# Optimization experiments

Hardware: AMD Instinct MI355X
Metric: run time of the kernel (lower is better)

## Reference

```python
import jax, jax.numpy as jnp
import numpy as np

N, F_IN, H, OUT, E = 50000, 128, 128, 40, 800000


def setup_inputs() -> dict:
    key = jax.random.key(0)
    ks = jax.random.split(key, 20)
    s = 0.05
    return {
        "x": jax.random.normal(ks[0], (N, F_IN), jnp.float32),
        "edge_index": jax.random.randint(ks[1], (2, E), 0, N, jnp.int64),
        # GATConv (heads=1)
        "W_gat": jax.random.normal(ks[2], (F_IN, H), jnp.float32) * s,
        "att_src": jax.random.normal(ks[3], (H,), jnp.float32) * s,
        "att_dst": jax.random.normal(ks[4], (H,), jnp.float32) * s,
        "b_gat": jnp.zeros((H,), jnp.float32),
        # GCNConv
        "W_gcn": jax.random.normal(ks[5], (F_IN, H), jnp.float32) * s,
        "b_gcn": jnp.zeros((H,), jnp.float32),
        # SAGEConv (mean aggr): lin_l on neighbors (with bias), lin_r on root (no bias)
        "W_sage_l": jax.random.normal(ks[6], (F_IN, H), jnp.float32) * s,
        "b_sage_l": jnp.zeros((H,), jnp.float32),
        "W_sage_r": jax.random.normal(ks[7], (F_IN, H), jnp.float32) * s,
        # MLP head
        "W1": jax.random.normal(ks[8], (3 * H, 2 * H), jnp.float32) * s,
        "b1": jnp.zeros((2 * H,), jnp.float32),
        "W2": jax.random.normal(ks[9], (2 * H, H), jnp.float32) * s,
        "b2": jnp.zeros((H,), jnp.float32),
        "W3": jax.random.normal(ks[10], (H, OUT), jnp.float32) * s,
        "b3": jnp.zeros((OUT,), jnp.float32),
        # BatchNorm1d(3H)
        "gamma": jnp.ones((3 * H,), jnp.float32),
        "beta": jnp.zeros((3 * H,), jnp.float32),
    }


def _add_self_loops(edge_index, n):
    loop = jnp.arange(n, dtype=edge_index.dtype)
    src = jnp.concatenate([edge_index[0], loop])
    dst = jnp.concatenate([edge_index[1], loop])
    return src, dst


def _gat(x, src, dst, n, W, att_src, att_dst, bias):
    h = x @ W                                   # [N, H]
    a_s = h @ att_src                           # [N]
    a_d = h @ att_dst                           # [N]
    e = jax.nn.leaky_relu(a_s[src] + a_d[dst], 0.2)  # [E']
    m = jax.ops.segment_max(e, dst, num_segments=n)
    ex = jnp.exp(e - m[dst])
    denom = jax.ops.segment_sum(ex, dst, num_segments=n)
    alpha = ex / denom[dst]
    out = jax.ops.segment_sum(alpha[:, None] * h[src], dst, num_segments=n)
    return out + bias


def _gcn(x, src, dst, n, W, bias):
    h = x @ W
    deg = jax.ops.segment_sum(jnp.ones_like(dst, dtype=h.dtype), dst, num_segments=n)
    dinv = jnp.where(deg > 0, jax.lax.rsqrt(deg), 0.0)
    norm = dinv[src] * dinv[dst]                # [E']
    out = jax.ops.segment_sum(norm[:, None] * h[src], dst, num_segments=n)
    return out + bias


def _sage(x, src, dst, n, W_l, b_l, W_r):
    agg = jax.ops.segment_sum(x[src], dst, num_segments=n)
    cnt = jax.ops.segment_sum(jnp.ones_like(dst, dtype=x.dtype), dst, num_segments=n)
    mean = agg / jnp.maximum(cnt, 1.0)[:, None]
    return mean @ W_l + b_l + x @ W_r


def reference(x, edge_index, W_gat, att_src, att_dst, b_gat, W_gcn, b_gcn,
              W_sage_l, b_sage_l, W_sage_r, W1, b1, W2, b2, W3, b3, gamma, beta):
    n = x.shape[0]
    src, dst = edge_index[0], edge_index[1]          # SAGE: no self-loops
    src_sl, dst_sl = _add_self_loops(edge_index, n)  # GAT/GCN add self-loops

    x_gat = _gat(x, src_sl, dst_sl, n, W_gat, att_src, att_dst, b_gat)
    x_gcn = _gcn(x, src_sl, dst_sl, n, W_gcn, b_gcn)
    x_sage = _sage(x, src, dst, n, W_sage_l, b_sage_l, W_sage_r)

    h = jnp.concatenate([x_gat, x_gcn, x_sage], axis=1)  # [N, 3H]
    # BatchNorm1d (training-mode batch statistics; biased variance, eps=1e-5)
    mu = h.mean(axis=0)
    var = h.var(axis=0)
    h = (h - mu) * jax.lax.rsqrt(var + 1e-5) * gamma + beta
    # dropout is identity at inference
    h = jax.nn.relu(h) @ W1 + b1
    h = jax.nn.relu(h) @ W2 + b2
    h = jax.nn.relu(h) @ W3 + b3
    return h
```

## Files before the change

### kernel.cpp

```cpp
#include <hip/hip_runtime.h>
#include <cstdint>
#include <cstddef>

#define NN   50000
#define FIN  128
#define HD   128
#define EE   800000
#define C3   384
#define NOUT 40

#define NBLK ((NN + 127) / 128)

#define SPLIT_BLKS ((NN + 4) / 4)

#define NBUCK ((NN + 511) / 512)
#define BCAP  16384
#define BK_BLKS ((EE + 8191) / 8192)
#define SCAP  12288

#define RCAP      132
#define STORE_CAP 128
#define ZROW NN

#define LDSW 132

typedef __attribute__((ext_vector_type(8))) short s8v;
typedef __attribute__((ext_vector_type(4))) float f4v;
typedef __attribute__((ext_vector_type(8))) ushort u8v;

typedef const __attribute__((address_space(1))) unsigned int* guintp;
typedef __attribute__((address_space(3))) unsigned int* luintp;

static __device__ __forceinline__ void async_copy16(const void* g, void* l) {
    __builtin_amdgcn_global_load_lds((guintp)g, (luintp)l, 16, 0, 0);
}

static __device__ __forceinline__ float b2f(ushort u) {
    return __uint_as_float((unsigned)u << 16);
}
static __device__ __forceinline__ ushort f2b(float v) {
    unsigned u = __float_as_uint(v);
    unsigned r = u + 0x7fffu + ((u >> 16) & 1u);
    return (ushort)(r >> 16);
}

__global__ __launch_bounds__(256) void k_split_x_att(
    const float* __restrict__ x,
    const float* __restrict__ w_as, const float* __restrict__ w_ad,
    ushort* __restrict__ xb,
    float* __restrict__ a_s, float* __restrict__ a_d)
{
    int node = blockIdx.x * 4 + (threadIdx.x >> 6);
    if (node > NN) return;
    int lane = threadIdx.x & 63;
    size_t o = (size_t)node * 128 + lane * 2;
    if (node == NN) {
        ushort2 z; z.x = 0; z.y = 0;
        *(ushort2*)(xb + o) = z;
        return;
    }
    float2 v  = *(const float2*)(x + o);
    { ushort2 u; u.x = f2b(v.x); u.y = f2b(v.y); *(ushort2*)(xb + o) = u; }
    float2 w1 = *(const float2*)(w_as + lane * 2);
    float2 w2 = *(const float2*)(w_ad + lane * 2);
    float s1 = v.x * w1.x + v.y * w1.y;
    float s2 = v.x * w2.x + v.y * w2.y;
    #pragma unroll
    for (int off = 32; off; off >>= 1) {
        s1 += __shfl_down(s1, off);
        s2 += __shfl_down(s2, off);
    }
    if (lane == 0) { a_s[node] = s1; a_d[node] = s2; }
}

__global__ void k_splitw_all(
    const float* __restrict__ Wg, const float* __restrict__ Wc,
    const float* __restrict__ Wl, const float* __restrict__ Wr,
    const float* __restrict__ W1, const float* __restrict__ W2,
    const float* __restrict__ W3,
    const float* __restrict__ asv, const float* __restrict__ adv,
    float* __restrict__ w_as, float* __restrict__ w_ad,
    ushort* __restrict__ btg, ushort* __restrict__ btc,
    ushort* __restrict__ btsg,
    ushort* __restrict__ bt1, ushort* __restrict__ bt2,
    ushort* __restrict__ bt3)
{
    int ry = blockIdx.x;
    int t = threadIdx.x;
    if (ry == 816) {
        if (t < 128) {
            float s1 = 0.f, s2 = 0.f;
            for (int j = 0; j < 128; ++j) {
                float w = Wg[t * 128 + j];
                s1 += w * asv[j];
                s2 += w * adv[j];
            }
            w_as[t] = s1; w_ad[t] = s2;
        }
        return;
    }
    const float* W = nullptr; ushort* dh; int K, Nw, n;
    bool sage = false;
    if (ry < 128)      { n = ry;       K = 128; Nw = 128; W = Wg; dh = btg; }
    else if (ry < 256) { n = ry - 128; K = 128; Nw = 128; W = Wc; dh = btc; }
    else if (ry < 384) { n = ry - 256; K = 256; Nw = 128; sage = true; dh = btsg; }
    else if (ry < 640) { n = ry - 384; K = 384; Nw = 256; W = W1; dh = bt1; }
    else if (ry < 768) { n = ry - 640; K = 256; Nw = 128; W = W2; dh = bt2; }
    else               { n = ry - 768; K = 128; Nw = 40;  W = W3; dh = bt3; }
    for (int k = t; k < K; k += 256) {
        float v;
        if (sage) v = (k < 128) ? Wl[(size_t)k * 128 + n] : Wr[(size_t)(k - 128) * 128 + n];
        else      v = (n < Nw) ? W[(size_t)k * Nw + n] : 0.f;
        dh[(size_t)n * K + k] = f2b(v);
    }
}

template<int NT, int NCH, int AX>
__global__ __launch_bounds__(256, 5) void k_gemm2(
    const ushort* __restrict__ A, int K,
    const ushort* __restrict__ Bt,
    int M, int mode,
    const float* __restrict__ bias,
    float* __restrict__ Cf, int ldc,
    ushort* __restrict__ Ch, int ldch,
    int colmax)
{
    constexpr int COLS = NT * 16;
    constexpr int HOPU = 8 * COLS;
    constexpr int KTOT = NCH * 128;

    __shared__ __align__(16) ushort S[16384];
    ushort* Bs = S;
    ushort* As = S + 8192;

    const int lane = threadIdx.x & 63;
    const int wave = threadIdx.x >> 6;
    const int quad = lane >> 4;
    const int ln15 = lane & 15;
    const int brow = AX ? blockIdx.y : blockIdx.x;
    const int bcol = AX ? blockIdx.x : blockIdx.y;
    const int row0 = brow * 128 + wave * 32;
    const int col0 = bcol * COLS;
    const int Rbase = brow * 128;

    auto stageB = [&](int c, int h) {
        for (int u0 = wave * 64; u0 < HOPU; u0 += 256) {
            int u  = u0 + lane;
            int kq  = u / COLS;
            int col = u - kq * COLS;
            int kk  = c * 128 + h * 64 + kq * 8;
            const ushort* gp = Bt + (size_t)(col0 + col) * KTOT + kk;
            async_copy16(gp, (char*)Bs + (size_t)u0 * 16);
        }
    };
    auto stageA = [&](int c, int h) {
        #pragma unroll
        for (int i = 0; i < 4; ++i) {
            int u0 = (wave * 4 + i) * 64;
            int u  = u0 + lane;
            int row = u >> 3;
            int s   = u & 7;
            int sg  = s ^ (row & 7);
            int rr = Rbase + row; if (rr > M - 1) rr = M - 1;
            int kk = c * 128 + h * 64 + sg * 8;
            const ushort* gp = A + (size_t)rr * K + kk;
            async_copy16(gp, (char*)As + (size_t)u0 * 16);
        }
    };
    auto afrag = [&](int jj, int mt) -> s8v {
        int r = wave * 32 + mt * 16 + ln15;
        int sg = jj * 4 + quad;
        int unit = r * 8 + (sg ^ (r & 7));
        return *(const s8v*)(As + (size_t)unit * 8);
    };

    f4v acc[2][NT] = {};

    auto compute = [&](int jj) {
        s8v a0 = afrag(jj, 0);
        s8v a1 = afrag(jj, 1);
        #pragma unroll
        for (int t = 0; t < NT; ++t) {
            int ub = (jj * 4 + quad) * COLS + t * 16 + ln15;
            s8v b = *(const s8v*)(Bs + (size_t)ub * 8);
            acc[0][t] = __builtin_amdgcn_mfma_f32_16x16x32_bf16(a0, b, acc[0][t], 0, 0, 0);
            acc[1][t] = __builtin_amdgcn_mfma_f32_16x16x32_bf16(a1, b, acc[1][t], 0, 0, 0);
        }
    };

    stageB(0, 0); stageA(0, 0);
    __syncthreads();

    #pragma unroll
    for (int ph = 0; ph < NCH; ++ph) {
        #pragma unroll
        for (int h = 0; h < 2; ++h) {
            compute(0); compute(1);
            if (!(ph == NCH - 1 && h == 1)) {
                __syncthreads();
                int nc = ph, nh = h + 1;
                if (nh == 2) { nh = 0; ++nc; }
                stageB(nc, nh); stageA(nc, nh);
                __syncthreads();
            }
        }
    }

    if (NT == 8 && mode == 0) {
        __syncthreads();
        ushort* Lp = S + wave * 2176;
        #pragma unroll
        for (int mt = 0; mt < 2; ++mt) {
            #pragma unroll
            for (int t = 0; t < NT; ++t) {
                int cc = col0 + t * 16 + ln15;
                #pragma unroll
                for (int r = 0; r < 4; ++r) {
                    float v = acc[mt][t][r] + bias[cc];
                    v = v > 0.f ? v : 0.f;
                    Lp[(quad * 4 + r) * LDSW + t * 16 + ln15] = f2b(v);
                }
            }
            int cb = (lane & 31) * 4;
            #pragma unroll
            for (int it = 0; it < 8; ++it) {
                int row2 = it * 2 + (lane >> 5);
                int rr = row0 + mt * 16 + row2;
                uint2 v = *(uint2*)(Lp + row2 * LDSW + cb);
                if (rr < M)
                    *(uint2*)(Ch + (size_t)rr * ldch + col0 + cb) = v;
            }
        }
    } else {
        #pragma unroll
        for (int t = 0; t < NT; ++t) {
            int cc = col0 + t * 16 + ln15;
            #pragma unroll
            for (int mt = 0; mt < 2; ++mt) {
                #pragma unroll
                for (int r = 0; r < 4; ++r) {
                    int rr = row0 + mt * 16 + quad * 4 + r;
                    if (rr < M && cc < colmax)
                        Cf[(size_t)rr * ldc + cc] = acc[mt][t][r] + bias[cc];
                }
            }
        }
    }
}

__global__ __launch_bounds__(256, 3) void k_gemm_prod(
    const ushort* __restrict__ tgb, const ushort* __restrict__ tcb,
    const ushort* __restrict__ tsb, const ushort* __restrict__ xb,
    const ushort* __restrict__ btg, const ushort* __restrict__ btc,
    const ushort* __restrict__ btsg,
    const float* __restrict__ bg, const float* __restrict__ bc,
    const float* __restrict__ bsl,
    float* __restrict__ pS, float* __restrict__ pQ,
    ushort* __restrict__ hch)
{
    constexpr int COLS = 128;
    constexpr int HOPU = 8 * COLS;
    __shared__ __align__(16) ushort S[16384];
    ushort* Bs = S;
    ushort* As = S + 8192;
    float* red = (float*)(S + 14336);

    const int z = blockIdx.z;
    const ushort* A1 = (z == 0) ? tgb : (z == 1) ? tcb : tsb;
    const ushort* Bt = (z == 0) ? btg : (z == 1) ? btc : btsg;
    const float*  bias = (z == 0) ? bg : (z == 1) ? bc : bsl;
    const int nch = (z == 2) ? 2 : 1;
    const int ktot = nch * 128;

    const int lane = threadIdx.x & 63;
    const int wave = threadIdx.x >> 6;
    const int quad = lane >> 4;
    const int ln15 = lane & 15;
    const int row0 = blockIdx.x * 128 + wave * 32;
    const int Rbase = blockIdx.x * 128;

    auto stageB = [&](int c, int h) {
        for (int u0 = wave * 64; u0 < HOPU; u0 += 256) {
            int u  = u0 + lane;
            int kq  = u / COLS;
            int col = u - kq * COLS;
            int kk  = c * 128 + h * 64 + kq * 8;
            const ushort* gp = Bt + (size_t)col * ktot + kk;
            async_copy16(gp, (char*)Bs + (size_t)u0 * 16);
        }
    };
    auto stageA = [&](int c, int h) {
        #pragma unroll
        for (int i = 0; i < 4; ++i) {
            int u0 = (wave * 4 + i) * 64;
            int u  = u0 + lane;
            int row = u >> 3;
            int s   = u & 7;
            int sg  = s ^ (row & 7);
            int rr = Rbase + row; if (rr > NN - 1) rr = NN - 1;
            int kk = c * 128 + h * 64 + sg * 8;
            const ushort* gp = (kk < 128) ? (A1 + (size_t)rr * 128 + kk)
                                          : (xb + (size_t)rr * 128 + (kk - 128));
            async_copy16(gp, (char*)As + (size_t)u0 * 16);
        }
    };
    auto afrag = [&](int jj, int mt) -> s8v {
        int r = wave * 32 + mt * 16 + ln15;
        int sg = jj * 4 + quad;
        int unit = r * 8 + (sg ^ (r & 7));
        return *(const s8v*)(As + (size_t)unit * 8);
    };

    f4v acc[2][8] = {};

    auto compute = [&](int jj) {
        s8v a0 = afrag(jj, 0);
        s8v a1 = afrag(jj, 1);
        #pragma unroll
        for (int t = 0; t < 8; ++t) {
            int ub = (jj * 4 + quad) * COLS + t * 16 + ln15;
            s8v b = *(const s8v*)(Bs + (size_t)ub * 8);
            acc[0][t] = __builtin_amdgcn_mfma_f32_16x16x32_bf16(a0, b, acc[0][t], 0, 0, 0);
            acc[1][t] = __builtin_amdgcn_mfma_f32_16x16x32_bf16(a1, b, acc[1][t], 0, 0, 0);
        }
    };

    stageB(0, 0); stageA(0, 0);
    __syncthreads();

    for (int ph = 0; ph < nch; ++ph) {
        for (int h = 0; h < 2; ++h) {
            compute(0); compute(1);
            if (!(ph == nch - 1 && h == 1)) {
                __syncthreads();
                int nc = ph, nh = h + 1;
                if (nh == 2) { nh = 0; ++nc; }
                stageB(nc, nh); stageA(nc, nh);
                __syncthreads();
            }
        }
    }

    __syncthreads();
    if (threadIdx.x < 256) red[threadIdx.x] = 0.f;
    ushort* Lp = S + wave * 2176;
    float sp[8] = {}, qp[8] = {};
    #pragma unroll
    for (int mt = 0; mt < 2; ++mt) {
        #pragma unroll
        for (int t = 0; t < 8; ++t) {
            #pragma unroll
            for (int r = 0; r < 4; ++r) {
                int rr = row0 + mt * 16 + quad * 4 + r;
                float v = acc[mt][t][r] + bias[t * 16 + ln15];
                Lp[(quad * 4 + r) * LDSW + t * 16 + ln15] = f2b(v);
                if (rr < NN) { sp[t] += v; qp[t] += v * v; }
            }
        }
        int cb = (lane & 31) * 4;
        #pragma unroll
        for (int it = 0; it < 8; ++it) {
            int row2 = it * 2 + (lane >> 5);
            int rr = row0 + mt * 16 + row2;
            uint2 v = *(uint2*)(Lp + row2 * LDSW + cb);
            if (rr < NN)
                *(uint2*)(hch + (size_t)rr * C3 + z * 128 + cb) = v;
        }
    }
    __syncthreads();
    #pragma unroll
    for (int t = 0; t < 8; ++t) {
        float s = sp[t], q = qp[t];
        s += __shfl_xor(s, 16); s += __shfl_xor(s, 32);
        q += __shfl_xor(q, 16); q += __shfl_xor(q, 32);
        if (quad == 0) {
            atomicAdd(&red[t * 16 + ln15], s);
            atomicAdd(&red[128 + t * 16 + ln15], q);
        }
    }
    __syncthreads();
    if (threadIdx.x < 128) {
        size_t o = (size_t)blockIdx.x * C3 + z * 128 + threadIdx.x;
        pS[o] = red[threadIdx.x];
        pQ[o] = red[128 + threadIdx.x];
    }
}

__global__ __launch_bounds__(1024) void k_bucket(
    const int* __restrict__ e_src, const int* __restrict__ e_dst,
    int* __restrict__ bcnt, uint* __restrict__ ebuf)
{
    __shared__ uint sval[8192];
    __shared__ int scnt[NBUCK], sbase[NBUCK];
    int t = threadIdx.x;
    if (t < NBUCK) scnt[t] = 0;
    __syncthreads();
    int e0 = blockIdx.x * 8192;
    #pragma unroll
    for (int i = 0; i < 8; ++i) {
        int g = e0 + i * 1024 + t;
        uint val = 0xffffffffu;
        if (g < EE) {
            int d = e_dst[g];
            int s = e_src[g];
            int b = d >> 9;
            val = ((uint)b << 25) | ((uint)(d & 511) << 16) | (uint)s;
            atomicAdd(&scnt[b], 1);
        }
        sval[i * 1024 + t] = val;
    }
    __syncthreads();
    if (t < NBUCK) {
        sbase[t] = atomicAdd(&bcnt[t], scnt[t]);
        scnt[t] = 0;
    }
    __syncthreads();
    #pragma unroll
    for (int i = 0; i < 8; ++i) {
        uint val = sval[i * 1024 + t];
        if (val != 0xffffffffu) {
            int b = val >> 25;
            int lo = atomicAdd(&scnt[b], 1);
            ebuf[(size_t)b * BCAP + sbase[b] + lo] = val;
        }
    }
}

__global__ __launch_bounds__(1024) void k_degscan(
    const int* __restrict__ bcnt, const uint* __restrict__ ebuf,
    int* __restrict__ offs, float* __restrict__ dinv)
{
    __shared__ int hist[512];
    __shared__ int sh[256];
    __shared__ int btop;
    int b = blockIdx.x, t = threadIdx.x;
    int d0 = b * 512;
    if (t < 512) hist[t] = 0;
    __syncthreads();
    int nb = bcnt[b];
    const uint* eb = ebuf + (size_t)b * BCAP;
    for (int i = t; i < nb; i += 1024)
        atomicAdd(&hist[(eb[i] >> 16) & 511], 1);
    __syncthreads();
    if (t < 64) {
        int acc = 0;
        for (int i = t; i < b; i += 64) {
            int nd = NN - i * 512; if (nd > 512) nd = 512;
            acc += bcnt[i] + nd;
        }
        #pragma unroll
        for (int off = 32; off; off >>= 1) acc += __shfl_down(acc, off);
        if (t == 0) btop = acc;
    }
    int v0 = 0, v1 = 0;
    if (t < 256) {
        int i0g = d0 + t * 2;
        v0 = (i0g < NN) ? hist[t * 2] + 1 : 0;
        v1 = (i0g + 1 < NN) ? hist[t * 2 + 1] + 1 : 0;
        sh[t] = v0 + v1;
    }
    __syncthreads();
    for (int off = 1; off < 256; off <<= 1) {
        int u = 0;
        if (t < 256 && t >= off) u = sh[t - off];
        __syncthreads();
        if (t < 256) sh[t] += u;
        __syncthreads();
    }
    if (t < 256) {
        int pair = v0 + v1;
        int excl = sh[t] - pair + btop;
        int i0g = d0 + t * 2;
        if (i0g < NN)     { offs[i0g] = excl;          dinv[i0g] = rsqrtf((float)v0); }
        if (i0g + 1 < NN) { offs[i0g + 1] = excl + v0; dinv[i0g + 1] = rsqrtf((float)v1); }
        if (b == NBUCK - 1 && t == 255) offs[NN] = excl + pair;
    }
}

__global__ __launch_bounds__(1024) void k_csr_build(
    const int* __restrict__ bcnt, const uint* __restrict__ ebuf,
    const int* __restrict__ offs, ushort* __restrict__ esrc)
{
    __shared__ ushort sout[SCAP];
    __shared__ int cur[512];
    int b = blockIdx.x, t = threadIdx.x;
    int d0 = b * 512;
    int ndst = NN - d0; if (ndst > 512) ndst = 512;
    int obase = offs[d0];
    if (t < ndst) cur[t] = offs[d0 + t] - obase;
    __syncthreads();
    int nb = bcnt[b];
    const uint* eb = ebuf + (size_t)b * BCAP;
    for (int i = t; i < nb; i += 1024) {
        uint val = eb[i];
        int slot = atomicAdd(&cur[(val >> 16) & 511], 1);
        sout[slot] = (ushort)(val & 0xffffu);
    }
    if (t < ndst) {
        int slot = atomicAdd(&cur[t], 1);
        sout[slot] = (ushort)(d0 + t);
    }
    __syncthreads();
    int total = offs[d0 + ndst] - obase;
    for (int i = t; i < total; i += 1024)
        esrc[obase + i] = sout[i];
}

__global__ __launch_bounds__(256) void k_gather(
    const ushort* __restrict__ esrc, const int* __restrict__ offs,
    const float* __restrict__ a_s, const float* __restrict__ a_d,
    const float* __restrict__ dinv,
    const ushort* __restrict__ xb,
    ushort* __restrict__ tgb, ushort* __restrict__ tcb,
    ushort* __restrict__ tsb)
{
    __shared__ uint2 recs[16][RCAP];
    int t = threadIdx.x;
    int qid = t >> 4;
    int ln = t & 15;
    int d = blockIdx.x * 16 + qid;
    if (d >= NN) return;
    uint2* rec = recs[qid];
    int beg = offs[d], end = offs[d + 1];
    int cnt = end - beg;
    float ad = a_d[d], dd = dinv[d];
    int stored = cnt < STORE_CAP ? cnt : STORE_CAP;

    float mloc = -3.0e38f;
    for (int b = 0; b < cnt; b += 16) {
        int j = b + ln;
        if (j < cnt) {
            int s = esrc[beg + j];
            float e = a_s[s] + ad;
            e = (e > 0.f) ? e : 0.2f * e;
            mloc = fmaxf(mloc, e);
            if (j < STORE_CAP) {
                uint2 r;
                r.x = __float_as_uint(e);
                r.y = (uint)s | ((uint)f2b(dinv[s] * dd) << 16);
                rec[j] = r;
            }
        }
    }
    float m = mloc;
    #pragma unroll
    for (int off = 1; off < 16; off <<= 1) m = fmaxf(m, __shfl_xor(m, off, 16));

    float denl = 0.f;
    for (int j = ln; j < stored; j += 16) {
        float ex = expf(__uint_as_float(rec[j].x) - m);
        denl += ex;
        rec[j].x = __float_as_uint(ex);
    }
    for (int idx = beg + STORE_CAP + ln; idx < end; idx += 16) {
        int s = esrc[idx];
        float e = a_s[s] + ad;
        e = (e > 0.f) ? e : 0.2f * e;
        denl += expf(e - m);
    }
    float den = denl;
    #pragma unroll
    for (int off = 1; off < 16; off <<= 1) den += __shfl_xor(den, off, 16);
    float rden = 1.f / den;

    for (int j = ln; j < stored; j += 16) {
        uint2 r = rec[j];
        uint2 q;
        q.x = (uint)f2b(__uint_as_float(r.x) * rden) | (r.y & 0xffff0000u);
        q.y = r.y & 0xffffu;
        rec[j] = q;
    }
    if (ln < 2) { uint2 q; q.x = 0u; q.y = (uint)ZROW; rec[stored + ln] = q; }

    float tg[8] = {}, tc[8] = {}, ts[8] = {};
    const ushort* xbs = xb + ln * 8;
    auto ldx = [&](uint srow) -> u8v {
        return *(const u8v*)(xbs + (size_t)srow * 128);
    };
    auto fmacc = [&](u8v x8, uint pw) {
        float wg = __uint_as_float(pw << 16);
        float wc = __uint_as_float(pw & 0xffff0000u);
        #pragma unroll
        for (int k = 0; k < 8; ++k) {
            float xv = b2f(x8[k]);
            tg[k] += wg * xv;
            tc[k] += wc * xv;
            ts[k] += xv;
        }
    };

    int Pcnt = (stored + 1) & ~1;
    uint2 rA = rec[0]; u8v xA = ldx(rA.y);
    uint2 rB; u8v xB;
    int j = 0;
    for (;;) {
        rB = rec[j + 1]; xB = ldx(rB.y);
        fmacc(xA, rA.x);
        if (++j >= Pcnt) break;
        rA = rec[j + 1]; xA = ldx(rA.y);
        fmacc(xB, rB.x);
        if (++j >= Pcnt) break;
    }

    for (int base = beg + STORE_CAP; base < end; base += 16) {
        int idx = base + ln;
        int s = ZROW; uint pw = 0;
        if (idx < end) {
            int ss = esrc[idx];
            float e = a_s[ss] + ad;
            e = (e > 0.f) ? e : 0.2f * e;
            pw = (uint)f2b(expf(e - m) * rden) | ((uint)f2b(dinv[ss] * dd) << 16);
            s = ss;
        }
        int cb = end - base; if (cb > 16) cb = 16;
        for (int jj = 0; jj < cb; ++jj) {
            int sa = __shfl(s, jj, 16);
            uint pa = (uint)__shfl((int)pw, jj, 16);
            fmacc(ldx((uint)sa), pa);
        }
    }

    u8v xd = *(const u8v*)(xb + (size_t)d * 128 + ln * 8);
    int cs = cnt - 1;
    float rc = 1.f / (float)(cs > 1 ? cs : 1);
    u8v og, oc, os;
    #pragma unroll
    for (int k = 0; k < 8; ++k) {
        og[k] = f2b(tg[k]);
        oc[k] = f2b(tc[k]);
        os[k] = f2b((ts[k] - b2f(xd[k])) * rc);
    }
    size_t row = (size_t)d * 128 + ln * 8;
    *(u8v*)(tgb + row) = og;
    *(u8v*)(tcb + row) = oc;
    *(u8v*)(tsb + row) = os;
}

__global__ void k_bn_final(const float* __restrict__ pS, const float* __restrict__ pQ,
                           const float* __restrict__ gamma, const float* __restrict__ beta,
                           float* __restrict__ scale, float* __restrict__ shift)
{
    int j = blockIdx.x * 64 + threadIdx.x;
    if (j >= C3) return;
    float s = 0.f, q = 0.f;
    for (int r = 0; r < NBLK; ++r) {
        s += pS[(size_t)r * C3 + j];
        q += pQ[(size_t)r * C3 + j];
    }
    const float rn = 1.f / (float)NN;
    float mu  = s * rn;
    float var = q * rn - mu * mu;
    float sc  = gamma[j] * rsqrtf(var + 1e-5f);
    scale[j] = sc;
    shift[j] = beta[j] - mu * sc;
}

__global__ __launch_bounds__(256) void k_bnrelu(
    ushort* __restrict__ hch,
    const float* __restrict__ scale, const float* __restrict__ shift)
{
    int p = blockIdx.x * blockDim.x + threadIdx.x;
    if (p >= NN * 48) return;
    int cidx = (p % 48) * 8;
    size_t o = (size_t)p * 8;
    uint4 w = *(uint4*)(hch + o);
    uint wr[4] = {w.x, w.y, w.z, w.w};
    uint out[4];
    #pragma unroll
    for (int i = 0; i < 4; ++i) {
        ushort u0 = (ushort)(wr[i] & 0xffffu), u1 = (ushort)(wr[i] >> 16);
        int cc = cidx + i * 2;
        float v0 = b2f(u0) * scale[cc]     + shift[cc];
        float v1 = b2f(u1) * scale[cc + 1] + shift[cc + 1];
        v0 = v0 > 0.f ? v0 : 0.f;
        v1 = v1 > 0.f ? v1 : 0.f;
        out[i] = (uint)f2b(v0) | ((uint)f2b(v1) << 16);
    }
    uint4 r; r.x = out[0]; r.y = out[1]; r.z = out[2]; r.w = out[3];
    *(uint4*)(hch + o) = r;
}

extern "C" void kernel_launch(void* const* d_in, const int* in_sizes, int n_in,
                              void* d_out, int out_size, void* d_ws, size_t ws_size,
                              hipStream_t stream) {
    const float* x        = (const float*)d_in[0];
    const int*   ei       = (const int*)d_in[1];
    const float* W_gat    = (const float*)d_in[2];
    const float* att_src  = (const float*)d_in[3];
    const float* att_dst  = (const float*)d_in[4];
    const float* b_gat    = (const float*)d_in[5];
    const float* W_gcn    = (const float*)d_in[6];
    const float* b_gcn    = (const float*)d_in[7];
    const float* W_sage_l = (const float*)d_in[8];
    const float* b_sage_l = (const float*)d_in[9];
    const float* W_sage_r = (const float*)d_in[10];
    const float* W1       = (const float*)d_in[11];
    const float* b1       = (const float*)d_in[12];
    const float* W2       = (const float*)d_in[13];
    const float* b2       = (const float*)d_in[14];
    const float* W3       = (const float*)d_in[15];
    const float* b3       = (const float*)d_in[16];
    const float* gamma    = (const float*)d_in[17];
    const float* beta     = (const float*)d_in[18];

    const int* e_src = ei;
    const int* e_dst = ei + EE;

    char* base = (char*)d_ws;
    size_t o = 0;
    ushort* hch  = (ushort*)(base + o); o += (size_t)NN * C3 * 2;
    ushort* tgb  = (ushort*)(base + o); o += (size_t)NN * 128 * 2;
    ushort* tcb  = (ushort*)(base + o); o += (size_t)NN * 128 * 2;
    ushort* tsb  = (ushort*)(base + o); o += (size_t)NN * 128 * 2;
    ushort* xb   = (ushort*)(base + o); o += (size_t)(NN + 1) * 128 * 2;
    ushort* esrc = (ushort*)(base + o); o += ((size_t)(EE + NN) * 2 + 15) & ~15ull;
    int*    offs = (int*)(base + o);    o += (size_t)(NN + 16) * 4;
    float*  as_  = (float*)(base + o);  o += (size_t)NN * 4;
    float*  ad_  = (float*)(base + o);  o += (size_t)NN * 4;
    float*  dinv = (float*)(base + o);  o += (size_t)NN * 4;
    int*    bcnt = (int*)(base + o);    o += 128 * 4;
    float*  pS   = (float*)(base + o);  o += (size_t)NBLK * C3 * 4;
    float*  pQ   = (float*)(base + o);  o += (size_t)NBLK * C3 * 4;
    float*  scale= (float*)(base + o);  o += C3 * 4;
    float*  shift= (float*)(base + o);  o += C3 * 4;
    float*  w_as = (float*)(base + o);  o += 128 * 4;
    float*  w_ad = (float*)(base + o);  o += 128 * 4;
    ushort* btg  = (ushort*)(base + o); o += 128 * 128 * 2;
    ushort* btc  = (ushort*)(base + o); o += 128 * 128 * 2;
    ushort* btsg = (ushort*)(base + o); o += 128 * 256 * 2;
    ushort* bt1  = (ushort*)(base + o); o += 256 * 384 * 2;
    ushort* bt2  = (ushort*)(base + o); o += 128 * 256 * 2;
    ushort* bt3  = (ushort*)(base + o); o += 48 * 128 * 2;
    ushort* a1 = tgb;
    ushort* a2 = tsb;
    uint*   ebuf = (uint*)hch;

    hipMemsetAsync(bcnt, 0, 128 * 4, stream);

    k_splitw_all<<<817, 256, 0, stream>>>(W_gat, W_gcn, W_sage_l, W_sage_r, W1, W2, W3,
        att_src, att_dst, w_as, w_ad, btg, btc, btsg, bt1, bt2, bt3);
    k_split_x_att<<<SPLIT_BLKS, 256, 0, stream>>>(x, w_as, w_ad, xb, as_, ad_);

    k_bucket<<<BK_BLKS, 1024, 0, stream>>>(e_src, e_dst, bcnt, ebuf);
    k_degscan<<<NBUCK, 1024, 0, stream>>>(bcnt, ebuf, offs, dinv);
    k_csr_build<<<NBUCK, 1024, 0, stream>>>(bcnt, ebuf, offs, esrc);

    k_gather<<<(NN + 15) / 16, 256, 0, stream>>>(
        esrc, offs, as_, ad_, dinv, xb, tgb, tcb, tsb);

    k_gemm_prod<<<dim3(NBLK, 1, 3), 256, 0, stream>>>(
        tgb, tcb, tsb, xb, btg, btc, btsg,
        b_gat, b_gcn, b_sage_l, pS, pQ, hch);

    k_bn_final<<<6, 64, 0, stream>>>(pS, pQ, gamma, beta, scale, shift);
    k_bnrelu<<<(NN * 48 + 255) / 256, 256, 0, stream>>>(hch, scale, shift);

    k_gemm2<8, 3, 1><<<dim3(2, NBLK), 256, 0, stream>>>(
        hch, 384, bt1, NN, 0, b1, nullptr, 0, a1, 256, 256);
    k_gemm2<8, 2, 0><<<dim3(NBLK, 1), 256, 0, stream>>>(
        a1, 256, bt2, NN, 0, b2, nullptr, 0, a2, 128, 128);
    k_gemm2<3, 1, 0><<<dim3(NBLK, 1), 256, 0, stream>>>(
        a2, 128, bt3, NN, 2, b3, (float*)d_out, NOUT, nullptr, 0, NOUT);
}
```

Before: 326.5 us.

## Fuse BatchNorm+ReLU into first MLP GEMM A-load and deepen gather prefetch

Removes the standalone BN+ReLU pass over the N×384 activation by applying scale/shift/ReLU while staging A tiles in the first MLP GEMM, replacing the async global->LDS copy with a synchronous load, transform and LDS store for that GEMM. The gather loop is unrolled to process four edges per step, with four-wide double-buffered row prefetch, more padding records and an occupancy hint. Launch bounds change for the GEMM (5->4 waves per SIMD target). The fused path loses async copy overlap and raises register pressure, and the BN transform is recomputed by both column blocks.

After: 313.7 us. 1.04x faster.

```diff
diff --git a/kernel.cpp b/kernel.cpp
--- a/kernel.cpp
+++ b/kernel.cpp
@@ -18,7 +18,7 @@
 #define BK_BLKS ((EE + 8191) / 8192)
 #define SCAP  12288
 
-#define RCAP      132
+#define RCAP      136
 #define STORE_CAP 128
 #define ZROW NN
 
@@ -115,15 +115,16 @@
     }
 }
 
-template<int NT, int NCH, int AX>
-__global__ __launch_bounds__(256, 5) void k_gemm2(
+template<int NT, int NCH, int AX, int BN>
+__global__ __launch_bounds__(256, 4) void k_gemm2(
     const ushort* __restrict__ A, int K,
     const ushort* __restrict__ Bt,
     int M, int mode,
     const float* __restrict__ bias,
     float* __restrict__ Cf, int ldc,
     ushort* __restrict__ Ch, int ldch,
-    int colmax)
+    int colmax,
+    const float* __restrict__ bnscale, const float* __restrict__ bnshift)
 {
     constexpr int COLS = NT * 16;
     constexpr int HOPU = 8 * COLS;
@@ -163,8 +164,30 @@
             int sg  = s ^ (row & 7);
             int rr = Rbase + row; if (rr > M - 1) rr = M - 1;
             int kk = c * 128 + h * 64 + sg * 8;
-            const ushort* gp = A + (size_t)rr * K + kk;
-            async_copy16(gp, (char*)As + (size_t)u0 * 16);
+            if constexpr (BN) {
+                uint4 w4 = *(const uint4*)(A + (size_t)rr * K + kk);
+                float4 sca = *(const float4*)(bnscale + kk);
+                float4 scb = *(const float4*)(bnscale + kk + 4);
+                float4 sha = *(const float4*)(bnshift + kk);
+                float4 shb = *(const float4*)(bnshift + kk + 4);
+                float sc8[8] = {sca.x,sca.y,sca.z,sca.w,scb.x,scb.y,scb.z,scb.w};
+                float sh8[8] = {sha.x,sha.y,sha.z,sha.w,shb.x,shb.y,shb.z,shb.w};
+                uint wr[4] = {w4.x, w4.y, w4.z, w4.w};
+                uint outw[4];
+                #pragma unroll
+                for (int p = 0; p < 4; ++p) {
+                    float v0 = b2f((ushort)(wr[p] & 0xffffu)) * sc8[p*2]   + sh8[p*2];
+                    float v1 = b2f((ushort)(wr[p] >> 16))     * sc8[p*2+1] + sh8[p*2+1];
+                    v0 = v0 > 0.f ? v0 : 0.f;
+                    v1 = v1 > 0.f ? v1 : 0.f;
+                    outw[p] = (uint)f2b(v0) | ((uint)f2b(v1) << 16);
+                }
+                uint4 ov; ov.x = outw[0]; ov.y = outw[1]; ov.z = outw[2]; ov.w = outw[3];
+                *(uint4*)(As + (size_t)u * 8) = ov;
+            } else {
+                const ushort* gp = A + (size_t)rr * K + kk;
+                async_copy16(gp, (char*)As + (size_t)u0 * 16);
+            }
         }
     };
     auto afrag = [&](int jj, int mt) -> s8v {
@@ -506,7 +529,7 @@
         esrc[obase + i] = sout[i];
 }
 
-__global__ __launch_bounds__(256) void k_gather(
+__global__ __launch_bounds__(256, 6) void k_gather(
     const ushort* __restrict__ esrc, const int* __restrict__ offs,
     const float* __restrict__ a_s, const float* __restrict__ a_d,
     const float* __restrict__ dinv,
@@ -570,7 +593,7 @@
         q.y = r.y & 0xffffu;
         rec[j] = q;
     }
-    if (ln < 2) { uint2 q; q.x = 0u; q.y = (uint)ZROW; rec[stored + ln] = q; }
+    if (ln < 8) { uint2 q; q.x = 0u; q.y = (uint)ZROW; rec[stored + ln] = q; }
 
     float tg[8] = {}, tc[8] = {}, ts[8] = {};
     const ushort* xbs = xb + ln * 8;
@@ -589,17 +612,32 @@
         }
     };
 
-    int Pcnt = (stored + 1) & ~1;
-    uint2 rA = rec[0]; u8v xA = ldx(rA.y);
-    uint2 rB; u8v xB;
+    int P4 = (stored + 3) & ~3;
+    uint pa0, pa1, pa2, pa3, pb0, pb1, pb2, pb3;
+    u8v xa0, xa1, xa2, xa3, ya0, ya1, ya2, ya3;
+    {
+        uint2 r0 = rec[0], r1 = rec[1], r2 = rec[2], r3 = rec[3];
+        pa0 = r0.x; xa0 = ldx(r0.y);
+        pa1 = r1.x; xa1 = ldx(r1.y);
+        pa2 = r2.x; xa2 = ldx(r2.y);
+        pa3 = r3.x; xa3 = ldx(r3.y);
+    }
     int j = 0;
     for (;;) {
-        rB = rec[j + 1]; xB = ldx(rB.y);
-        fmacc(xA, rA.x);
-        if (++j >= Pcnt) break;
-        rA = rec[j + 1]; xA = ldx(rA.y);
-        fmacc(xB, rB.x);
-        if (++j >= Pcnt) break;
+        { uint2 r0 = rec[j+4], r1 = rec[j+5], r2 = rec[j+6], r3 = rec[j+7];
+          pb0 = r0.x; ya0 = ldx(r0.y);
+          pb1 = r1.x; ya1 = ldx(r1.y);
+          pb2 = r2.x; ya2 = ldx(r2.y);
+          pb3 = r3.x; ya3 = ldx(r3.y); }
+        fmacc(xa0, pa0); fmacc(xa1, pa1); fmacc(xa2, pa2); fmacc(xa3, pa3);
+        j += 4; if (j >= P4) break;
+        { uint2 r0 = rec[j+4], r1 = rec[j+5], r2 = rec[j+6], r3 = rec[j+7];
+          pa0 = r0.x; xa0 = ldx(r0.y);
+          pa1 = r1.x; xa1 = ldx(r1.y);
+          pa2 = r2.x; xa2 = ldx(r2.y);
+          pa3 = r3.x; xa3 = ldx(r3.y); }
+        fmacc(ya0, pb0); fmacc(ya1, pb1); fmacc(ya2, pb2); fmacc(ya3, pb3);
+        j += 4; if (j >= P4) break;
     }
 
     for (int base = beg + STORE_CAP; base < end; base += 16) {
@@ -653,31 +691,6 @@
     float sc  = gamma[j] * rsqrtf(var + 1e-5f);
     scale[j] = sc;
     shift[j] = beta[j] - mu * sc;
-}
-
-__global__ __launch_bounds__(256) void k_bnrelu(
-    ushort* __restrict__ hch,
-    const float* __restrict__ scale, const float* __restrict__ shift)
-{
-    int p = blockIdx.x * blockDim.x + threadIdx.x;
-    if (p >= NN * 48) return;
-    int cidx = (p % 48) * 8;
-    size_t o = (size_t)p * 8;
-    uint4 w = *(uint4*)(hch + o);
-    uint wr[4] = {w.x, w.y, w.z, w.w};
-    uint out[4];
-    #pragma unroll
-    for (int i = 0; i < 4; ++i) {
-        ushort u0 = (ushort)(wr[i] & 0xffffu), u1 = (ushort)(wr[i] >> 16);
-        int cc = cidx + i * 2;
-        float v0 = b2f(u0) * scale[cc]     + shift[cc];
-        float v1 = b2f(u1) * scale[cc + 1] + shift[cc + 1];
-        v0 = v0 > 0.f ? v0 : 0.f;
-        v1 = v1 > 0.f ? v1 : 0.f;
-        out[i] = (uint)f2b(v0) | ((uint)f2b(v1) << 16);
-    }
-    uint4 r; r.x = out[0]; r.y = out[1]; r.z = out[2]; r.w = out[3];
-    *(uint4*)(hch + o) = r;
 }
 
 extern "C" void kernel_launch(void* const* d_in, const int* in_sizes, int n_in,
@@ -753,12 +766,11 @@
         b_gat, b_gcn, b_sage_l, pS, pQ, hch);
 
     k_bn_final<<<6, 64, 0, stream>>>(pS, pQ, gamma, beta, scale, shift);
-    k_bnrelu<<<(NN * 48 + 255) / 256, 256, 0, stream>>>(hch, scale, shift);
-
-    k_gemm2<8, 3, 1><<<dim3(2, NBLK), 256, 0, stream>>>(
-        hch, 384, bt1, NN, 0, b1, nullptr, 0, a1, 256, 256);
-    k_gemm2<8, 2, 0><<<dim3(NBLK, 1), 256, 0, stream>>>(
-        a1, 256, bt2, NN, 0, b2, nullptr, 0, a2, 128, 128);
-    k_gemm2<3, 1, 0><<<dim3(NBLK, 1), 256, 0, stream>>>(
-        a2, 128, bt3, NN, 2, b3, (float*)d_out, NOUT, nullptr, 0, NOUT);
-}
+
+    k_gemm2<8, 3, 1, 1><<<dim3(2, NBLK), 256, 0, stream>>>(
+        hch, 384, bt1, NN, 0, b1, nullptr, 0, a1, 256, 256, scale, shift);
+    k_gemm2<8, 2, 0, 0><<<dim3(NBLK, 1), 256, 0, stream>>>(
+        a1, 256, bt2, NN, 0, b2, nullptr, 0, a2, 128, 128, nullptr, nullptr);
+    k_gemm2<3, 1, 0, 0><<<dim3(NBLK, 1), 256, 0, stream>>>(
+        a2, 128, bt3, NN, 2, b3, (float*)d_out, NOUT, nullptr, 0, NOUT, nullptr, nullptr);
+}
```
